# Performance work log

Hardware: AMD Instinct MI355X
Metric: run time of the kernel (lower is better)

## Reference

```python
import jax, jax.numpy as jnp
import numpy as np

N, C, V, T = 256, 256, 25, 20
K = 3            # kernel_size
PAD = 1          # padding
O = 256          # out_channels
C4 = C // 4
EPS = 1e-5


def _bn(x, p, axes_shape):
    # p: (4, dim) = gamma, beta, running_mean, running_var (eval-mode BN)
    g, b, m, v = (p[i].reshape(axes_shape) for i in range(4))
    return (x - m) * (g / jnp.sqrt(v + EPS)) + b


def setup_inputs() -> dict:
    key = jax.random.key(0)
    ks = jax.random.split(key, 12)
    rn = lambda k, s, sc=0.05: jax.random.normal(k, s, jnp.float32) * sc
    bn = lambda k, d: jnp.stack([
        1.0 + 0.1 * jax.random.normal(jax.random.fold_in(k, 0), (d,), jnp.float32),  # gamma
        0.1 * jax.random.normal(jax.random.fold_in(k, 1), (d,), jnp.float32),        # beta
        0.1 * jax.random.normal(jax.random.fold_in(k, 2), (d,), jnp.float32),        # mean
        0.5 + jax.random.uniform(jax.random.fold_in(k, 3), (d,), jnp.float32),       # var
    ])
    return {
        "x": jax.random.normal(ks[0], (N, C, V, T), jnp.float32),
        "Wg1": rn(ks[1], (2 * T, T), 0.2),      # Linear T -> 2T (no bias)
        "Wg2": rn(ks[2], (K, 2 * T), 0.2),      # Linear 2T -> K (no bias)
        "Wl1": rn(ks[3], (C4, C, K)),           # Conv1d C -> C/4, kernel K
        "Wl2": rn(ks[4], (C, C4)),              # Conv1d C/4 -> C, kernel 1
        "Wc2": rn(ks[5], (O, C)),               # 1x1 Conv2d C -> O (no bias)
        "bng": bn(ks[6], 2 * T),
        "bnl": bn(ks[7], C4),
        "bn1p": bn(ks[8], C),
        "bn2p": bn(ks[9], O),
    }


def reference(x, Wg1, Wg2, Wl1, Wl2, Wc2, bng, bnl, bn1p, bn2p):
    n, c, v, t = x.shape
    new_x = jnp.transpose(x, (0, 1, 3, 2))            # (N, C, T, V)
    pooled = new_x.mean(axis=-1)                       # (N, C, T)  adaptive_avg_pool over V

    # --- G branch: per-(n,c) dynamic temporal kernel ---
    h = pooled.reshape(n * c, t) @ Wg1.T               # (NC, 2T)
    h = jax.nn.relu(_bn(h, bng, (1, 2 * t)))
    kern = jax.nn.softmax(h @ Wg2.T, axis=-1)          # (NC, K)
    kern = kern.reshape(n, c, K)

    # --- L branch: local temporal excitation ---
    l = jax.lax.conv_general_dilated(
        pooled, Wl1, window_strides=(1,), padding=[(K // 2, K // 2)],
        dimension_numbers=("NCH", "OIH", "NCH"))      # (N, C4, T)
    l = jax.nn.relu(_bn(l, bnl, (1, C4, 1)))
    l = jax.nn.sigmoid(jnp.einsum("oc,nct->not", Wl2, l))  # (N, C, T)
    new_x = new_x + l[..., None]                       # (N, C, T, V)

    # --- dynamic depthwise temporal conv (groups = N*C) ---
    padded = jnp.pad(new_x, ((0, 0), (0, 0), (PAD, PAD), (0, 0)))
    out = sum(kern[:, :, k, None, None] * padded[:, :, k:k + t, :] for k in range(K))

    out = jnp.transpose(out, (0, 1, 3, 2))             # (N, C, V, T)
    out = jax.nn.relu(_bn(out, bn1p, (1, c, 1, 1)))    # bn1 + relu; dropout in eval = identity
    out = jnp.einsum("oc,ncvt->novt", Wc2, out)        # 1x1 conv
    out = jax.nn.relu(_bn(out, bn2p, (1, O, 1, 1)))    # bn2 + relu
    return out
```

## Files before the change

kernel.cpp:

```cpp
#include <hip/hip_runtime.h>
#include <hip/hip_bf16.h>
#include <math.h>

#define N_ 256
#define C_ 256
#define V_ 25
#define T_ 20
#define C4_ 64
#define O_ 256
#define VT_ 500
#define EPS_ 1e-5f

typedef unsigned short ushort_t;
typedef unsigned short us4 __attribute__((ext_vector_type(4)));
typedef short short8 __attribute__((ext_vector_type(8)));
typedef float f32x4 __attribute__((ext_vector_type(4)));

__device__ __forceinline__ float bf2f(ushort_t u) {
    unsigned int v = ((unsigned int)u) << 16;
    return __builtin_bit_cast(float, v);
}
__device__ __forceinline__ ushort_t f2bf(float f) {
    unsigned int u = __builtin_bit_cast(unsigned int, f);
    unsigned int r = u + 0x7fffu + ((u >> 16) & 1u);
    return (ushort_t)(r >> 16);
}

__global__ __launch_bounds__(256) void k_pool(const float* __restrict__ x,
                                              float* __restrict__ pooled,
                                              const float* __restrict__ Wc2,
                                              ushort_t* __restrict__ wbf) {
    int tid = threadIdx.x;
    if (blockIdx.x >= 8192) {
        int i = (blockIdx.x - 8192) * 256 + tid;
        f32x4 v = ((const f32x4*)Wc2)[i];
        us4 o; o.x = f2bf(v.x); o.y = f2bf(v.y); o.z = f2bf(v.z); o.w = f2bf(v.w);
        ((us4*)wbf)[i] = o;
        return;
    }
    __shared__ float xs[8][504];
    const f32x4* src = (const f32x4*)(x + (size_t)blockIdx.x * 8 * VT_);
    for (int i = tid; i < 1000; i += 256) {
        int r = i / 125, cidx = (i % 125) * 4;
        *(f32x4*)&xs[r][cidx] = src[i];
    }
    __syncthreads();
    if (tid < 160) {
        int r = tid / 20, t = tid % 20;
        float s = 0.f;
#pragma unroll
        for (int v = 0; v < V_; ++v) s += xs[r][v * T_ + t];
        pooled[blockIdx.x * 160 + tid] = s * 0.04f;
    }
}

__global__ __launch_bounds__(256) void k_gl(const float* __restrict__ pooled,
                                            const float* __restrict__ Wg1,
                                            const float* __restrict__ Wg2,
                                            const float* __restrict__ Wl1,
                                            const float* __restrict__ Wl2,
                                            const float* __restrict__ bng,
                                            const float* __restrict__ bnl,
                                            float* __restrict__ kern,
                                            float* __restrict__ l2out) {
    __shared__ float pp[C_][22];
    __shared__ float wg1[800];
    __shared__ float wg2[120];
    __shared__ float sg[40], bg[40];
    __shared__ float ls[C4_][20];
    __shared__ float sl[C4_], bl[C4_];
    int tid = threadIdx.x;
    int n = blockIdx.x;

    for (int i = tid; i < 800; i += 256) wg1[i] = Wg1[i];
    if (tid < 120) wg2[tid] = Wg2[tid];
    if (tid < 40) {
        float g = bng[tid], b = bng[40 + tid];
        float m = bng[80 + tid], v = bng[120 + tid];
        float s = g * rsqrtf(v + EPS_);
        sg[tid] = s; bg[tid] = b - m * s;
    }
    if (tid < C4_) {
        float g = bnl[tid], b = bnl[64 + tid];
        float m = bnl[128 + tid], v = bnl[192 + tid];
        float s = g * rsqrtf(v + EPS_);
        sl[tid] = s; bl[tid] = b - m * s;
    }
    {
        const f32x4* pn = (const f32x4*)(pooled + n * (C_ * T_));
#pragma unroll
        for (int q = 0; q < 5; ++q) {
            int id = q * 256 + tid;
            int c = id / 5, qq = id % 5;
            f32x4 v = pn[id];
            pp[c][qq * 4 + 1] = v.x; pp[c][qq * 4 + 2] = v.y;
            pp[c][qq * 4 + 3] = v.z; pp[c][qq * 4 + 4] = v.w;
        }
        pp[tid][0] = 0.f; pp[tid][21] = 0.f;
    }
    __syncthreads();

    {
        int c = tid;
        float p[20];
#pragma unroll
        for (int t = 0; t < 20; ++t) p[t] = pp[c][t + 1];
        float l0 = 0.f, l1 = 0.f, l2 = 0.f;
#pragma unroll 4
        for (int j = 0; j < 40; ++j) {
            float h = 0.f;
#pragma unroll
            for (int t = 0; t < 20; ++t) h = fmaf(wg1[j * 20 + t], p[t], h);
            h = fmaxf(fmaf(h, sg[j], bg[j]), 0.f);
            l0 = fmaf(wg2[j], h, l0);
            l1 = fmaf(wg2[40 + j], h, l1);
            l2 = fmaf(wg2[80 + j], h, l2);
        }
        float mx = fmaxf(l0, fmaxf(l1, l2));
        float e0 = __expf(l0 - mx), e1 = __expf(l1 - mx), e2 = __expf(l2 - mx);
        float inv = 1.f / (e0 + e1 + e2);
        float* kp = kern + (n * C_ + c) * 3;
        kp[0] = e0 * inv; kp[1] = e1 * inv; kp[2] = e2 * inv;
    }

    {
        int c4 = tid >> 2;
        int t0 = (tid & 3) * 5;
        float acc0 = 0.f, acc1 = 0.f, acc2 = 0.f, acc3 = 0.f, acc4 = 0.f;
        const float* w = Wl1 + c4 * (C_ * 3);
#pragma unroll 8
        for (int c = 0; c < C_; ++c) {
            float w0 = w[c * 3 + 0];
            float w1 = w[c * 3 + 1];
            float w2 = w[c * 3 + 2];
            float a0 = pp[c][t0 + 0], a1 = pp[c][t0 + 1], a2 = pp[c][t0 + 2];
            float a3 = pp[c][t0 + 3], a4 = pp[c][t0 + 4], a5 = pp[c][t0 + 5];
            float a6 = pp[c][t0 + 6];
            acc0 = fmaf(w0, a0, fmaf(w1, a1, fmaf(w2, a2, acc0)));
            acc1 = fmaf(w0, a1, fmaf(w1, a2, fmaf(w2, a3, acc1)));
            acc2 = fmaf(w0, a2, fmaf(w1, a3, fmaf(w2, a4, acc2)));
            acc3 = fmaf(w0, a3, fmaf(w1, a4, fmaf(w2, a5, acc3)));
            acc4 = fmaf(w0, a4, fmaf(w1, a5, fmaf(w2, a6, acc4)));
        }
        float s = sl[c4], b = bl[c4];
        ls[c4][t0 + 0] = fmaxf(fmaf(acc0, s, b), 0.f);
        ls[c4][t0 + 1] = fmaxf(fmaf(acc1, s, b), 0.f);
        ls[c4][t0 + 2] = fmaxf(fmaf(acc2, s, b), 0.f);
        ls[c4][t0 + 3] = fmaxf(fmaf(acc3, s, b), 0.f);
        ls[c4][t0 + 4] = fmaxf(fmaf(acc4, s, b), 0.f);
    }
    __syncthreads();

    {
        int c = tid;
        float acc[20];
#pragma unroll
        for (int t = 0; t < 20; ++t) acc[t] = 0.f;
        const float* w = Wl2 + c * C4_;
#pragma unroll 4
        for (int c4 = 0; c4 < C4_; ++c4) {
            float wv = w[c4];
#pragma unroll
            for (int t = 0; t < 20; ++t) acc[t] = fmaf(wv, ls[c4][t], acc[t]);
        }
        f32x4* o = (f32x4*)(l2out + (n * C_ + c) * T_);
#pragma unroll
        for (int q = 0; q < 5; ++q) {
            f32x4 v;
            v.x = 1.f / (1.f + __expf(-acc[q*4+0]));
            v.y = 1.f / (1.f + __expf(-acc[q*4+1]));
            v.z = 1.f / (1.f + __expf(-acc[q*4+2]));
            v.w = 1.f / (1.f + __expf(-acc[q*4+3]));
            o[q] = v;
        }
    }
}

#define YSTRIDE 264

__global__ __launch_bounds__(256, 2) void k_main(const float* __restrict__ x,
                                                 const ushort_t* __restrict__ wbf,
                                                 const float* __restrict__ bn1p,
                                                 const float* __restrict__ bn2p,
                                                 const float* __restrict__ kern,
                                                 const float* __restrict__ l2g,
                                                 float* __restrict__ out) {
    __shared__ __align__(16) char smem[61184];
    ushort_t* yT  = (ushort_t*)smem;
    float*    outs = (float*)smem;
    float* s2t = (float*)(smem + 59136);
    float* b2t = (float*)(smem + 60160);

    int tid = threadIdx.x;
    int n = blockIdx.y;
    int vblk = blockIdx.x;
    const float* xn = x + n * (C_ * V_ * T_);

    float s1, b1, k0, k1, k2, l2r[20];
    {
        int c = tid;
        float g1 = bn1p[c], be1 = bn1p[256 + c];
        float m1 = bn1p[512 + c], v1 = bn1p[768 + c];
        s1 = g1 * rsqrtf(v1 + EPS_);
        b1 = be1 - m1 * s1;
        float g2 = bn2p[c], be2 = bn2p[256 + c];
        float m2 = bn2p[512 + c], v2 = bn2p[768 + c];
        float s2 = g2 * rsqrtf(v2 + EPS_);
        s2t[c] = s2; b2t[c] = be2 - m2 * s2;
        const float* kp = kern + (n * C_ + c) * 3;
        k0 = kp[0]; k1 = kp[1]; k2 = kp[2];
        const f32x4* lp = (const f32x4*)(l2g + (n * C_ + c) * T_);
#pragma unroll
        for (int q = 0; q < 5; ++q) {
            f32x4 v = lp[q];
            l2r[q*4+0] = v.x; l2r[q*4+1] = v.y; l2r[q*4+2] = v.z; l2r[q*4+3] = v.w;
        }
    }

    for (int vl = 0; vl < 5; ++vl) {
        ushort_t* xs = yT + (vl * 20) * YSTRIDE;
#pragma unroll
        for (int q = 0; q < 5; ++q) {
            int id = q * 256 + tid;
            int c = id / 5, qq = id % 5;
            f32x4 v = *(const f32x4*)(xn + c * VT_ + vblk * 100 + vl * 20 + qq * 4);
            us4 o; o.x = f2bf(v.x); o.y = f2bf(v.y); o.z = f2bf(v.z); o.w = f2bf(v.w);
            *(us4*)(xs + c * 20 + qq * 4) = o;
        }
        __syncthreads();
        float a[22];
        a[0] = 0.f; a[21] = 0.f;
        {
            const ushort_t* xrow = xs + tid * 20;
#pragma unroll
            for (int qq = 0; qq < 5; ++qq) {
                us4 u = *(const us4*)(xrow + qq * 4);
                a[qq*4 + 1] = bf2f(u.x) + l2r[qq*4 + 0];
                a[qq*4 + 2] = bf2f(u.y) + l2r[qq*4 + 1];
                a[qq*4 + 3] = bf2f(u.z) + l2r[qq*4 + 2];
                a[qq*4 + 4] = bf2f(u.w) + l2r[qq*4 + 3];
            }
        }
        __syncthreads();
        {
            ushort_t* yrow = yT + (vl * 20) * YSTRIDE + tid;
#pragma unroll
            for (int t = 0; t < 20; ++t) {
                float z = fmaf(k0, a[t], fmaf(k1, a[t + 1], k2 * a[t + 2]));
                yrow[t * YSTRIDE] = f2bf(fmaxf(fmaf(z, s1, b1), 0.f));
            }
        }
    }
    for (int i = tid; i < 12 * YSTRIDE; i += 256) yT[100 * YSTRIDE + i] = 0;
    __syncthreads();

    int lane = tid & 63;
    int wave = tid >> 6;
    int mrow = lane & 15;
    int kof = (lane >> 4) * 8;
    int prow = (lane >> 4) * 4;
    int obase = wave * 64;

    f32x4 acc[4][7];
#pragma unroll
    for (int mt = 0; mt < 4; ++mt)
#pragma unroll
        for (int ct = 0; ct < 7; ++ct) acc[mt][ct] = (f32x4){0.f, 0.f, 0.f, 0.f};

#pragma unroll 2
    for (int kk = 0; kk < C_; kk += 32) {
        short8 af[4];
        short8 bfr[7];
#pragma unroll
        for (int mt = 0; mt < 4; ++mt)
            af[mt] = *(const short8*)(wbf + (obase + mt * 16 + mrow) * C_ + kk + kof);
#pragma unroll
        for (int ct = 0; ct < 7; ++ct)
            bfr[ct] = *(const short8*)(yT + (ct * 16 + mrow) * YSTRIDE + kk + kof);
#pragma unroll
        for (int mt = 0; mt < 4; ++mt)
#pragma unroll
            for (int ct = 0; ct < 7; ++ct)
                acc[mt][ct] = __builtin_amdgcn_mfma_f32_16x16x32_bf16(af[mt], bfr[ct], acc[mt][ct], 0, 0, 0);
    }
    __syncthreads();

    float* outn = out + n * (O_ * VT_);
#pragma unroll
    for (int P = 0; P < 2; ++P) {
#pragma unroll
        for (int mtl = 0; mtl < 2; ++mtl) {
            int mt = 2 * P + mtl;
#pragma unroll
            for (int ct = 0; ct < 7; ++ct) {
                int pl = ct * 16 + mrow;
                if (pl < 100) {
#pragma unroll
                    for (int r = 0; r < 4; ++r) {
                        int og = obase + mt * 16 + prow + r;
                        int oo = wave * 32 + mtl * 16 + prow + r;
                        outs[oo * 100 + pl] =
                            fmaxf(fmaf(acc[mt][ct][r], s2t[og], b2t[og]), 0.f);
                    }
                }
            }
        }
        __syncthreads();
        for (int i = tid; i < 3200; i += 256) {
            int oo = i / 25, col = i % 25;
            int og = (oo >> 5) * 64 + P * 32 + (oo & 31);
            *(f32x4*)(outn + og * VT_ + vblk * 100 + col * 4) = ((const f32x4*)outs)[i];
        }
        __syncthreads();
    }
}

extern "C" void kernel_launch(void* const* d_in, const int* in_sizes, int n_in,
                              void* d_out, int out_size, void* d_ws, size_t ws_size,
                              hipStream_t stream) {
    const float* x   = (const float*)d_in[0];
    const float* Wg1 = (const float*)d_in[1];
    const float* Wg2 = (const float*)d_in[2];
    const float* Wl1 = (const float*)d_in[3];
    const float* Wl2 = (const float*)d_in[4];
    const float* Wc2 = (const float*)d_in[5];
    const float* bng = (const float*)d_in[6];
    const float* bnl = (const float*)d_in[7];
    const float* bn1p = (const float*)d_in[8];
    const float* bn2p = (const float*)d_in[9];
    float* out = (float*)d_out;

    float* ws = (float*)d_ws;
    float* pooled = ws;
    float* kern   = ws + 1310720;
    float* l2g    = ws + 1310720 + 196608;
    ushort_t* wbf = (ushort_t*)(ws + 1310720 + 196608 + 1310720);

    k_pool<<<dim3(8256), dim3(256), 0, stream>>>(x, pooled, Wc2, wbf);
    k_gl<<<dim3(N_), dim3(256), 0, stream>>>(pooled, Wg1, Wg2, Wl1, Wl2, bng, bnl, kern, l2g);
    k_main<<<dim3(5, N_), dim3(256), 0, stream>>>(x, wbf, bn1p, bn2p, kern, l2g, out);
}
```

Measured before the change: 363.9 us.

## Split main GEMM into two register-light passes, store output directly, prefetch x

Splits the 7 column-tile MFMA accumulation into two passes (4 tiles then 3, with an overlapping tile at 84 so no padded rows are needed). This cuts accumulator registers and the LDS footprint so launch bounds can target 3 blocks per CU. The epilogue now writes BN2+ReLU results straight to global memory, with scale and bias fetched by lane shuffles instead of LDS staging. The x loads are software-prefetched one slab ahead and barriers use a lightweight LDS-only wait. In exchange the weight fragments are reloaded twice and the direct stores are scalar and less coalesced than the old vectorised write-out.

```diff
diff --git a/kernel.cpp b/kernel.cpp
--- a/kernel.cpp
+++ b/kernel.cpp
@@ -24,6 +24,13 @@
     unsigned int u = __builtin_bit_cast(unsigned int, f);
     unsigned int r = u + 0x7fffu + ((u >> 16) & 1u);
     return (ushort_t)(r >> 16);
+}
+
+__device__ __forceinline__ void bar_lds() {
+    __builtin_amdgcn_sched_barrier(0);
+    asm volatile("s_waitcnt lgkmcnt(0)" ::: "memory");
+    __builtin_amdgcn_s_barrier();
+    __builtin_amdgcn_sched_barrier(0);
 }
 
 __global__ __launch_bounds__(256) void k_pool(const float* __restrict__ x,
@@ -178,25 +185,71 @@
 
 #define YSTRIDE 264
 
-__global__ __launch_bounds__(256, 2) void k_main(const float* __restrict__ x,
+template <int NT>
+__device__ __forceinline__ void gemm_pass(const ushort_t* __restrict__ yT,
+                                          const ushort_t* __restrict__ wbf,
+                                          float* __restrict__ outn,
+                                          const int (&ctb)[NT], int ov_idx,
+                                          int obase, int mrow, int kof, int prow,
+                                          float s2, float b2) {
+    f32x4 acc[4][NT];
+#pragma unroll
+    for (int mt = 0; mt < 4; ++mt)
+#pragma unroll
+        for (int j = 0; j < NT; ++j) acc[mt][j] = (f32x4){0.f, 0.f, 0.f, 0.f};
+
+#pragma unroll 1
+    for (int kk = 0; kk < C_; kk += 32) {
+        short8 af[4];
+        short8 bfr[NT];
+#pragma unroll
+        for (int mt = 0; mt < 4; ++mt)
+            af[mt] = *(const short8*)(wbf + (obase + mt * 16 + mrow) * C_ + kk + kof);
+#pragma unroll
+        for (int j = 0; j < NT; ++j)
+            bfr[j] = *(const short8*)(yT + (ctb[j] + mrow) * YSTRIDE + kk + kof);
+#pragma unroll
+        for (int mt = 0; mt < 4; ++mt)
+#pragma unroll
+            for (int j = 0; j < NT; ++j)
+                acc[mt][j] = __builtin_amdgcn_mfma_f32_16x16x32_bf16(af[mt], bfr[j], acc[mt][j], 0, 0, 0);
+    }
+
+#pragma unroll
+    for (int mt = 0; mt < 4; ++mt) {
+#pragma unroll
+        for (int r = 0; r < 4; ++r) {
+            int lsrc = mt * 16 + prow + r;
+            float s2w = __shfl(s2, lsrc);
+            float b2w = __shfl(b2, lsrc);
+            float* orow = outn + (size_t)(obase + lsrc) * VT_;
+#pragma unroll
+            for (int j = 0; j < NT; ++j) {
+                bool skip = (j == ov_idx) && (mrow < 12);
+                if (!skip) {
+                    float vr = fmaxf(fmaf(acc[mt][j][r], s2w, b2w), 0.f);
+                    orow[ctb[j] + mrow] = vr;
+                }
+            }
+        }
+    }
+}
+
+__global__ __launch_bounds__(256, 3) void k_main(const float* __restrict__ x,
                                                  const ushort_t* __restrict__ wbf,
                                                  const float* __restrict__ bn1p,
                                                  const float* __restrict__ bn2p,
                                                  const float* __restrict__ kern,
                                                  const float* __restrict__ l2g,
                                                  float* __restrict__ out) {
-    __shared__ __align__(16) char smem[61184];
-    ushort_t* yT  = (ushort_t*)smem;
-    float*    outs = (float*)smem;
-    float* s2t = (float*)(smem + 59136);
-    float* b2t = (float*)(smem + 60160);
+    __shared__ __align__(16) ushort_t yT[100 * YSTRIDE];
 
     int tid = threadIdx.x;
     int n = blockIdx.y;
     int vblk = blockIdx.x;
-    const float* xn = x + n * (C_ * V_ * T_);
-
-    float s1, b1, k0, k1, k2, l2r[20];
+    const float* xn = x + (size_t)n * (C_ * V_ * T_) + vblk * 100;
+
+    float s1, b1, k0, k1, k2, s2, b2, l2r[20];
     {
         int c = tid;
         float g1 = bn1p[c], be1 = bn1p[256 + c];
@@ -205,8 +258,8 @@
         b1 = be1 - m1 * s1;
         float g2 = bn2p[c], be2 = bn2p[256 + c];
         float m2 = bn2p[512 + c], v2 = bn2p[768 + c];
-        float s2 = g2 * rsqrtf(v2 + EPS_);
-        s2t[c] = s2; b2t[c] = be2 - m2 * s2;
+        s2 = g2 * rsqrtf(v2 + EPS_);
+        b2 = be2 - m2 * s2;
         const float* kp = kern + (n * C_ + c) * 3;
         k0 = kp[0]; k1 = kp[1]; k2 = kp[2];
         const f32x4* lp = (const f32x4*)(l2g + (n * C_ + c) * T_);
@@ -217,17 +270,34 @@
         }
     }
 
+    int offg[5], offs[5];
+#pragma unroll
+    for (int q = 0; q < 5; ++q) {
+        int id = q * 256 + tid;
+        int c = id / 5, qq = id % 5;
+        offg[q] = c * VT_ + qq * 4;
+        offs[q] = c * 20 + qq * 4;
+    }
+
+    f32x4 ld[5];
+#pragma unroll
+    for (int q = 0; q < 5; ++q) ld[q] = *(const f32x4*)(xn + offg[q]);
+
     for (int vl = 0; vl < 5; ++vl) {
-        ushort_t* xs = yT + (vl * 20) * YSTRIDE;
+        f32x4 ldn[5];
+        if (vl < 4) {
+#pragma unroll
+            for (int q = 0; q < 5; ++q)
+                ldn[q] = *(const f32x4*)(xn + offg[q] + (vl + 1) * 20);
+        }
+        ushort_t* xs = yT + vl * 20 * YSTRIDE;
 #pragma unroll
         for (int q = 0; q < 5; ++q) {
-            int id = q * 256 + tid;
-            int c = id / 5, qq = id % 5;
-            f32x4 v = *(const f32x4*)(xn + c * VT_ + vblk * 100 + vl * 20 + qq * 4);
-            us4 o; o.x = f2bf(v.x); o.y = f2bf(v.y); o.z = f2bf(v.z); o.w = f2bf(v.w);
-            *(us4*)(xs + c * 20 + qq * 4) = o;
-        }
-        __syncthreads();
+            us4 o; o.x = f2bf(ld[q].x); o.y = f2bf(ld[q].y);
+            o.z = f2bf(ld[q].z); o.w = f2bf(ld[q].w);
+            *(us4*)(xs + offs[q]) = o;
+        }
+        bar_lds();
         float a[22];
         a[0] = 0.f; a[21] = 0.f;
         {
@@ -241,18 +311,21 @@
                 a[qq*4 + 4] = bf2f(u.w) + l2r[qq*4 + 3];
             }
         }
-        __syncthreads();
+        bar_lds();
         {
-            ushort_t* yrow = yT + (vl * 20) * YSTRIDE + tid;
+            ushort_t* yrow = yT + vl * 20 * YSTRIDE + tid;
 #pragma unroll
             for (int t = 0; t < 20; ++t) {
                 float z = fmaf(k0, a[t], fmaf(k1, a[t + 1], k2 * a[t + 2]));
                 yrow[t * YSTRIDE] = f2bf(fmaxf(fmaf(z, s1, b1), 0.f));
             }
         }
-    }
-    for (int i = tid; i < 12 * YSTRIDE; i += 256) yT[100 * YSTRIDE + i] = 0;
-    __syncthreads();
+        if (vl < 4) {
+#pragma unroll
+            for (int q = 0; q < 5; ++q) ld[q] = ldn[q];
+        }
+    }
+    bar_lds();
 
     int lane = tid & 63;
     int wave = tid >> 6;
@@ -260,58 +333,15 @@
     int kof = (lane >> 4) * 8;
     int prow = (lane >> 4) * 4;
     int obase = wave * 64;
-
-    f32x4 acc[4][7];
-#pragma unroll
-    for (int mt = 0; mt < 4; ++mt)
-#pragma unroll
-        for (int ct = 0; ct < 7; ++ct) acc[mt][ct] = (f32x4){0.f, 0.f, 0.f, 0.f};
-
-#pragma unroll 2
-    for (int kk = 0; kk < C_; kk += 32) {
-        short8 af[4];
-        short8 bfr[7];
-#pragma unroll
-        for (int mt = 0; mt < 4; ++mt)
-            af[mt] = *(const short8*)(wbf + (obase + mt * 16 + mrow) * C_ + kk + kof);
-#pragma unroll
-        for (int ct = 0; ct < 7; ++ct)
-            bfr[ct] = *(const short8*)(yT + (ct * 16 + mrow) * YSTRIDE + kk + kof);
-#pragma unroll
-        for (int mt = 0; mt < 4; ++mt)
-#pragma unroll
-            for (int ct = 0; ct < 7; ++ct)
-                acc[mt][ct] = __builtin_amdgcn_mfma_f32_16x16x32_bf16(af[mt], bfr[ct], acc[mt][ct], 0, 0, 0);
-    }
-    __syncthreads();
-
-    float* outn = out + n * (O_ * VT_);
-#pragma unroll
-    for (int P = 0; P < 2; ++P) {
-#pragma unroll
-        for (int mtl = 0; mtl < 2; ++mtl) {
-            int mt = 2 * P + mtl;
-#pragma unroll
-            for (int ct = 0; ct < 7; ++ct) {
-                int pl = ct * 16 + mrow;
-                if (pl < 100) {
-#pragma unroll
-                    for (int r = 0; r < 4; ++r) {
-                        int og = obase + mt * 16 + prow + r;
-                        int oo = wave * 32 + mtl * 16 + prow + r;
-                        outs[oo * 100 + pl] =
-                            fmaxf(fmaf(acc[mt][ct][r], s2t[og], b2t[og]), 0.f);
-                    }
-                }
-            }
-        }
-        __syncthreads();
-        for (int i = tid; i < 3200; i += 256) {
-            int oo = i / 25, col = i % 25;
-            int og = (oo >> 5) * 64 + P * 32 + (oo & 31);
-            *(f32x4*)(outn + og * VT_ + vblk * 100 + col * 4) = ((const f32x4*)outs)[i];
-        }
-        __syncthreads();
+    float* outn = out + (size_t)n * (O_ * VT_) + vblk * 100;
+
+    {
+        const int ctb0[4] = {0, 16, 32, 48};
+        gemm_pass<4>(yT, wbf, outn, ctb0, -1, obase, mrow, kof, prow, s2, b2);
+    }
+    {
+        const int ctb1[3] = {64, 80, 84};
+        gemm_pass<3>(yT, wbf, outn, ctb1, 2, obase, mrow, kof, prow, s2, b2);
     }
 }
 
```

Measured after the change: 366.8 us. Within noise of the previous version (+0.8%).
